# Kernel tuning notes

Hardware: AMD Instinct MI355X
Metric: run time of the kernel (lower is better)

The kernel has to match this reference:

```python
import jax, jax.numpy as jnp
import numpy as np

B, N_IN, D = 2, 262144, 32
N_OUT, K, NK = 65536, 4, 9
MIN_DIST = 0.01


def setup_inputs() -> dict:
    key = jax.random.key(0)
    k1, k2, k3, k4 = jax.random.split(key, 4)
    x_level_in = jax.random.normal(k1, (B, N_IN, D), dtype=jnp.float32)
    coords_in = jax.random.uniform(k2, (2, B, N_IN), dtype=jnp.float32)
    coords_out = jax.random.uniform(k3, (2, B, N_OUT, K), dtype=jnp.float32)
    neighbor_idx = jax.random.randint(k4, (B, N_OUT, K, NK), 0, N_IN)
    sigma = jnp.ones((D,), dtype=jnp.float32) * (MIN_DIST * 200.0)
    return {
        "x_level_in": x_level_in,
        "coords_in": coords_in,
        "coords_out": coords_out,
        "sigma": sigma,
        "neighbor_idx": neighbor_idx,
    }


def reference(x_level_in, coords_in, coords_out, sigma, neighbor_idx):
    # x_level_in: [B, N_in, D]; coords_in: [2, B, N_in]
    # coords_out: [2, B, N_out, K]; neighbor_idx: [B, N_out, K, NK]; sigma: [D]
    b = jnp.arange(x_level_in.shape[0])[:, None, None, None]  # batch index broadcaster
    # gather neighbor coordinates across the input grid: [2, B, N_out, K, NK]
    nb_coords = coords_in[:, b, neighbor_idx]
    # squared euclidean distance in (lon, lat): [B, N_out, K, NK]
    d2 = jnp.sum((coords_out[..., None] - nb_coords) ** 2, axis=0)
    # per-channel Gaussian/RBF weights: [B, N_out, K, NK, D]
    w = jnp.exp(-d2[..., None] / (2.0 * sigma ** 2))
    # gather neighbor features: [B, N_out, K, NK, D]
    feats = x_level_in[b, neighbor_idx]
    # normalized weighted aggregate over the NK neighbors: [B, N_out, K, D]
    num = jnp.sum(w * feats, axis=3)
    den = jnp.sum(w, axis=3) + 1e-9
    x = num / den
    # flatten (N_out, K) -> sequence dim, as in forward's final view
    return x.reshape(x.shape[0], -1, x.shape[-1])
```

## Files before the change

kernel.cpp:

```cpp
#include <hip/hip_runtime.h>
#include <hip/hip_fp16.h>

constexpr int B        = 2;
constexpr int N_IN     = 262144;
constexpr int D        = 32;
constexpr int N_OUT    = 65536;
constexpr int K        = 4;
constexpr int NK       = 9;
constexpr int P        = B * N_OUT * K;
constexpr int PK_BITS  = 18;
constexpr size_t XTOT  = (size_t)B * N_IN * D;

typedef _Float16 half4v __attribute__((ext_vector_type(4)));
typedef _Float16 half8v __attribute__((ext_vector_type(8)));

__global__ __launch_bounds__(256) void cvt_fp16_kernel(
    const float* __restrict__ x, _Float16* __restrict__ xh)
{
    const size_t i = (size_t)(blockIdx.x * 256 + threadIdx.x) * 8;
    const float4 a = *reinterpret_cast<const float4*>(x + i);
    const float4 b = *reinterpret_cast<const float4*>(x + i + 4);
    half8v h;
    h[0] = (_Float16)a.x; h[1] = (_Float16)a.y;
    h[2] = (_Float16)a.z; h[3] = (_Float16)a.w;
    h[4] = (_Float16)b.x; h[5] = (_Float16)b.y;
    h[6] = (_Float16)b.z; h[7] = (_Float16)b.w;
    *reinterpret_cast<half8v*>(xh + i) = h;
}

__global__ __launch_bounds__(256) void projection_kernel_h(
    const _Float16* __restrict__ xh,
    const float* __restrict__ coords_in,
    const float* __restrict__ coords_out,
    const float* __restrict__ sigma,
    const int*   __restrict__ nidx,
    float*       __restrict__ out)
{
    const int tid   = blockIdx.x * 256 + threadIdx.x;
    const int point = tid >> 3;
    const int q     = tid & 7;

    const int b     = point >> PK_BITS;
    const int cbase = b * N_IN;

    const float cox = coords_out[point];
    const float coy = coords_out[P + point];

    const float4 sg = *reinterpret_cast<const float4*>(sigma + q * 4);
    const float s0 = 1.0f / (2.0f * sg.x * sg.x);
    const float s1 = 1.0f / (2.0f * sg.y * sg.y);
    const float s2 = 1.0f / (2.0f * sg.z * sg.z);
    const float s3 = 1.0f / (2.0f * sg.w * sg.w);

    float4 num = make_float4(0.f, 0.f, 0.f, 0.f);
    float4 den = make_float4(0.f, 0.f, 0.f, 0.f);

    const int* __restrict__ ip = nidx + (size_t)point * NK;

    #pragma unroll
    for (int nk = 0; nk < NK; ++nk) {
        const int idx = ip[nk];
        const float cx = coords_in[cbase + idx];
        const float cy = coords_in[B * N_IN + cbase + idx];
        const float dx = cox - cx;
        const float dy = coy - cy;
        const float d2 = dx * dx + dy * dy;

        const half4v f = *reinterpret_cast<const half4v*>(
            xh + (size_t)(cbase + idx) * D + q * 4);

        const float w0 = __expf(-d2 * s0);
        const float w1 = __expf(-d2 * s1);
        const float w2 = __expf(-d2 * s2);
        const float w3 = __expf(-d2 * s3);

        num.x += w0 * (float)f[0];  den.x += w0;
        num.y += w1 * (float)f[1];  den.y += w1;
        num.z += w2 * (float)f[2];  den.z += w2;
        num.w += w3 * (float)f[3];  den.w += w3;
    }

    float4 o;
    o.x = num.x / (den.x + 1e-9f);
    o.y = num.y / (den.y + 1e-9f);
    o.z = num.z / (den.z + 1e-9f);
    o.w = num.w / (den.w + 1e-9f);

    *reinterpret_cast<float4*>(out + (size_t)point * D + q * 4) = o;
}

__global__ __launch_bounds__(256) void projection_kernel_f32(
    const float* __restrict__ x,
    const float* __restrict__ coords_in,
    const float* __restrict__ coords_out,
    const float* __restrict__ sigma,
    const int*   __restrict__ nidx,
    float*       __restrict__ out)
{
    const int tid   = blockIdx.x * 256 + threadIdx.x;
    const int point = tid >> 3;
    const int q     = tid & 7;
    const int b     = point >> PK_BITS;
    const int cbase = b * N_IN;

    const float cox = coords_out[point];
    const float coy = coords_out[P + point];

    const float4 sg = *reinterpret_cast<const float4*>(sigma + q * 4);
    const float s0 = 1.0f / (2.0f * sg.x * sg.x);
    const float s1 = 1.0f / (2.0f * sg.y * sg.y);
    const float s2 = 1.0f / (2.0f * sg.z * sg.z);
    const float s3 = 1.0f / (2.0f * sg.w * sg.w);

    float4 num = make_float4(0.f, 0.f, 0.f, 0.f);
    float4 den = make_float4(0.f, 0.f, 0.f, 0.f);
    const int* __restrict__ ip = nidx + (size_t)point * NK;

    #pragma unroll
    for (int nk = 0; nk < NK; ++nk) {
        const int idx = ip[nk];
        const float cx = coords_in[cbase + idx];
        const float cy = coords_in[B * N_IN + cbase + idx];
        const float dx = cox - cx;
        const float dy = coy - cy;
        const float d2 = dx * dx + dy * dy;
        const float4 f = *reinterpret_cast<const float4*>(
            x + (size_t)(cbase + idx) * D + q * 4);
        const float w0 = __expf(-d2 * s0);
        const float w1 = __expf(-d2 * s1);
        const float w2 = __expf(-d2 * s2);
        const float w3 = __expf(-d2 * s3);
        num.x += w0 * f.x;  den.x += w0;
        num.y += w1 * f.y;  den.y += w1;
        num.z += w2 * f.z;  den.z += w2;
        num.w += w3 * f.w;  den.w += w3;
    }

    float4 o;
    o.x = num.x / (den.x + 1e-9f);
    o.y = num.y / (den.y + 1e-9f);
    o.z = num.z / (den.z + 1e-9f);
    o.w = num.w / (den.w + 1e-9f);
    *reinterpret_cast<float4*>(out + (size_t)point * D + q * 4) = o;
}

extern "C" void kernel_launch(void* const* d_in, const int* in_sizes, int n_in,
                              void* d_out, int out_size, void* d_ws, size_t ws_size,
                              hipStream_t stream) {
    const float* x      = (const float*)d_in[0];
    const float* cin    = (const float*)d_in[1];
    const float* cout_  = (const float*)d_in[2];
    const float* sigma  = (const float*)d_in[3];
    const int*   nidx   = (const int*)  d_in[4];
    float*       outp   = (float*)d_out;

    const int block = 256;
    const int grid_main = (P * 8) / block;

    if (ws_size >= XTOT * sizeof(_Float16)) {
        _Float16* xh = (_Float16*)d_ws;
        const int grid_cvt = (int)(XTOT / 8 / block);
        cvt_fp16_kernel<<<grid_cvt, block, 0, stream>>>(x, xh);
        projection_kernel_h<<<grid_main, block, 0, stream>>>(
            xh, cin, cout_, sigma, nidx, outp);
    } else {
        projection_kernel_f32<<<grid_main, block, 0, stream>>>(
            x, cin, cout_, sigma, nidx, outp);
    }
}
```

Before: 238.3 us.

## Pack input coords, batch gathers up front, XCD-aware block mapping, uniform-sigma fast path

Adds a kernel that interleaves the x and y input coordinates into float2, so each neighbor's coordinates come from one gather instead of two. The projection kernel now issues all index, coordinate and feature loads before any math, to raise memory-level parallelism. Blocks are remapped so each group of XCDs works on a single batch, aiming at better L2 locality. When the four sigmas a thread uses are equal, it computes one exp per neighbor instead of four. The extra pack kernel costs a pass over coords_in, and preloading everything raises register pressure.

```diff
diff --git a/kernel.cpp b/kernel.cpp
--- a/kernel.cpp
+++ b/kernel.cpp
@@ -8,7 +8,7 @@
 constexpr int K        = 4;
 constexpr int NK       = 9;
 constexpr int P        = B * N_OUT * K;
-constexpr int PK_BITS  = 18;
+constexpr int PPB      = N_OUT * K;
 constexpr size_t XTOT  = (size_t)B * N_IN * D;
 
 typedef _Float16 half4v __attribute__((ext_vector_type(4)));
@@ -28,20 +28,30 @@
     *reinterpret_cast<half8v*>(xh + i) = h;
 }
 
+__global__ __launch_bounds__(256) void pack_coords_kernel(
+    const float* __restrict__ cin, float2* __restrict__ cp)
+{
+    const int i = blockIdx.x * 256 + threadIdx.x;
+    cp[i] = make_float2(cin[i], cin[B * N_IN + i]);
+}
+
 __global__ __launch_bounds__(256) void projection_kernel_h(
     const _Float16* __restrict__ xh,
-    const float* __restrict__ coords_in,
-    const float* __restrict__ coords_out,
-    const float* __restrict__ sigma,
-    const int*   __restrict__ nidx,
-    float*       __restrict__ out)
-{
-    const int tid   = blockIdx.x * 256 + threadIdx.x;
-    const int point = tid >> 3;
-    const int q     = tid & 7;
-
-    const int b     = point >> PK_BITS;
-    const int cbase = b * N_IN;
+    const float2*   __restrict__ cpack,
+    const float*    __restrict__ coords_out,
+    const float*    __restrict__ sigma,
+    const int*      __restrict__ nidx,
+    float*          __restrict__ out)
+{
+    const int bid   = blockIdx.x;
+    const int xcd   = bid & 7;
+    const int j     = bid >> 3;
+    const int batch = xcd >> 2;
+    const int bbi   = j * 4 + (xcd & 3);
+    const int point = batch * PPB + bbi * 32 + (threadIdx.x >> 3);
+    const int q     = threadIdx.x & 7;
+
+    const int cbase = batch * N_IN;
 
     const float cox = coords_out[point];
     const float coy = coords_out[P + point];
@@ -51,33 +61,55 @@
     const float s1 = 1.0f / (2.0f * sg.y * sg.y);
     const float s2 = 1.0f / (2.0f * sg.z * sg.z);
     const float s3 = 1.0f / (2.0f * sg.w * sg.w);
+    const bool uni = (sg.x == sg.y) && (sg.y == sg.z) && (sg.z == sg.w);
+
+    int idxs[NK];
+    const int* __restrict__ ip = nidx + (size_t)point * NK;
+    #pragma unroll
+    for (int t = 0; t < NK; ++t) idxs[t] = ip[t];
+
+    float2 c[NK];
+    #pragma unroll
+    for (int t = 0; t < NK; ++t) c[t] = cpack[cbase + idxs[t]];
+
+    half4v f[NK];
+    #pragma unroll
+    for (int t = 0; t < NK; ++t)
+        f[t] = *reinterpret_cast<const half4v*>(
+            xh + (size_t)(cbase + idxs[t]) * D + q * 4);
 
     float4 num = make_float4(0.f, 0.f, 0.f, 0.f);
     float4 den = make_float4(0.f, 0.f, 0.f, 0.f);
 
-    const int* __restrict__ ip = nidx + (size_t)point * NK;
-
-    #pragma unroll
-    for (int nk = 0; nk < NK; ++nk) {
-        const int idx = ip[nk];
-        const float cx = coords_in[cbase + idx];
-        const float cy = coords_in[B * N_IN + cbase + idx];
-        const float dx = cox - cx;
-        const float dy = coy - cy;
-        const float d2 = dx * dx + dy * dy;
-
-        const half4v f = *reinterpret_cast<const half4v*>(
-            xh + (size_t)(cbase + idx) * D + q * 4);
-
-        const float w0 = __expf(-d2 * s0);
-        const float w1 = __expf(-d2 * s1);
-        const float w2 = __expf(-d2 * s2);
-        const float w3 = __expf(-d2 * s3);
-
-        num.x += w0 * (float)f[0];  den.x += w0;
-        num.y += w1 * (float)f[1];  den.y += w1;
-        num.z += w2 * (float)f[2];  den.z += w2;
-        num.w += w3 * (float)f[3];  den.w += w3;
+    if (uni) {
+        #pragma unroll
+        for (int t = 0; t < NK; ++t) {
+            const float dx = cox - c[t].x;
+            const float dy = coy - c[t].y;
+            const float d2 = dx * dx + dy * dy;
+            const float w  = __expf(-d2 * s0);
+            num.x += w * (float)f[t][0];
+            num.y += w * (float)f[t][1];
+            num.z += w * (float)f[t][2];
+            num.w += w * (float)f[t][3];
+            den.x += w;
+        }
+        den.y = den.x; den.z = den.x; den.w = den.x;
+    } else {
+        #pragma unroll
+        for (int t = 0; t < NK; ++t) {
+            const float dx = cox - c[t].x;
+            const float dy = coy - c[t].y;
+            const float d2 = dx * dx + dy * dy;
+            const float w0 = __expf(-d2 * s0);
+            const float w1 = __expf(-d2 * s1);
+            const float w2 = __expf(-d2 * s2);
+            const float w3 = __expf(-d2 * s3);
+            num.x += w0 * (float)f[t][0];  den.x += w0;
+            num.y += w1 * (float)f[t][1];  den.y += w1;
+            num.z += w2 * (float)f[t][2];  den.z += w2;
+            num.w += w3 * (float)f[t][3];  den.w += w3;
+        }
     }
 
     float4 o;
@@ -100,7 +132,7 @@
     const int tid   = blockIdx.x * 256 + threadIdx.x;
     const int point = tid >> 3;
     const int q     = tid & 7;
-    const int b     = point >> PK_BITS;
+    const int b     = point / PPB;
     const int cbase = b * N_IN;
 
     const float cox = coords_out[point];
@@ -157,12 +189,16 @@
     const int block = 256;
     const int grid_main = (P * 8) / block;
 
-    if (ws_size >= XTOT * sizeof(_Float16)) {
+    const size_t xh_bytes = XTOT * sizeof(_Float16);
+    const size_t cp_bytes = (size_t)B * N_IN * sizeof(float2);
+
+    if (ws_size >= xh_bytes + cp_bytes) {
         _Float16* xh = (_Float16*)d_ws;
-        const int grid_cvt = (int)(XTOT / 8 / block);
-        cvt_fp16_kernel<<<grid_cvt, block, 0, stream>>>(x, xh);
+        float2*   cp = (float2*)((char*)d_ws + xh_bytes);
+        cvt_fp16_kernel<<<(int)(XTOT / 8 / block), block, 0, stream>>>(x, xh);
+        pack_coords_kernel<<<(B * N_IN) / block, block, 0, stream>>>(cin, cp);
         projection_kernel_h<<<grid_main, block, 0, stream>>>(
-            xh, cin, cout_, sigma, nidx, outp);
+            xh, cp, cout_, sigma, nidx, outp);
     } else {
         projection_kernel_f32<<<grid_main, block, 0, stream>>>(
             x, cin, cout_, sigma, nidx, outp);
```

New measurement: 238.5 us. Within noise of the previous version (+0.1%).
